# Performance work log

Hardware: AMD Instinct MI355X
Metric: run time of the kernel (lower is better)

The kernel has to match this reference:

```python
import jax, jax.numpy as jnp
import numpy as np

EMBED = 768
HEADS = 12
FACTOR = 2
LN_EPS = 1e-5


def layer_norm(x, gamma, beta):
    mu = jnp.mean(x, axis=-1, keepdims=True)
    var = jnp.mean(jnp.square(x - mu), axis=-1, keepdims=True)
    return (x - mu) * jax.lax.rsqrt(var + LN_EPS) * gamma + beta


def setup_inputs() -> dict:
    key = jax.random.key(0)
    ks = jax.random.split(key, 8)
    B, S, E = 8, 1024, EMBED
    H = FACTOR * E
    s_e = 1.0 / np.sqrt(E)
    s_h = 1.0 / np.sqrt(H)
    return {
        "x": jax.random.normal(ks[0], (B, S, E), jnp.float32),
        "Wq": jax.random.normal(ks[1], (E, E), jnp.float32) * s_e,
        "Wk": jax.random.normal(ks[2], (E, E), jnp.float32) * s_e,
        "Wv": jax.random.normal(ks[3], (E, E), jnp.float32) * s_e,
        "W1": jax.random.normal(ks[4], (E, H), jnp.float32) * s_e,
        "b1": jnp.zeros((H,), jnp.float32),
        "W2": jax.random.normal(ks[5], (H, E), jnp.float32) * s_h,
        "b2": jnp.zeros((E,), jnp.float32),
        "g1": jnp.ones((E,), jnp.float32),
        "beta1": jnp.zeros((E,), jnp.float32),
        "g2": jnp.ones((E,), jnp.float32),
        "beta2": jnp.zeros((E,), jnp.float32),
    }


def reference(x, Wq, Wk, Wv, W1, b1, W2, b2, g1, beta1, g2, beta2):
    B, S, E = x.shape
    hd = E // HEADS
    # NOTE: original reshapes (B,S,E)->(B,H,S,hd) WITHOUT transposing heads
    # (non-standard: mixes sequence blocks across heads) - replicated faithfully.
    q = (x @ Wq).reshape(B, HEADS, S, hd)
    k = (x @ Wk).reshape(B, HEADS, S, hd)
    v = (x @ Wv).reshape(B, HEADS, S, hd)
    # no 1/sqrt(d) scaling in the original
    attn = jax.nn.softmax(jnp.einsum('bnqd,bnkd->bnqk', q, k), axis=-1)
    # NOTE: original einsum 'bnqk,bnvd->bnqd' sums over BOTH k and v
    # (value is sum-pooled over its sequence axis) - replicated faithfully.
    out = jnp.einsum('bnqk,bnvd->bnqd', attn, v)
    out = out.transpose(0, 2, 1, 3).reshape(B, S, E)
    a = x + layer_norm(out, g1, beta1)
    # GELU after BOTH linears (exact GELU, torch default)
    h = jax.nn.gelu(a @ W1 + b1, approximate=False)
    m = jax.nn.gelu(h @ W2 + b2, approximate=False)
    return x + layer_norm(m, g2, beta2)
```

## Files before the change

### kernel.cpp

```cpp
#include <hip/hip_runtime.h>
#include <hip/hip_bf16.h>
#include <math.h>

#define E_ 768
#define HID_ 1536
#define SQ_ 1024

typedef unsigned short u16;
using bf16x8 = __attribute__((ext_vector_type(8))) __bf16;
using f32x4  = __attribute__((ext_vector_type(4))) float;

__device__ __forceinline__ u16 f2bf(float f) {
  union { float f; unsigned u; } v; v.f = f;
  unsigned r = v.u + 0x7FFFu + ((v.u >> 16) & 1u);
  return (u16)(r >> 16);
}
__device__ __forceinline__ float bf2f(u16 h) {
  union { unsigned u; float f; } v; v.u = ((unsigned)h) << 16; return v.f;
}
__device__ __forceinline__ float gelu_f(float x) {
  return 0.5f * x * (1.0f + erff(x * 0.70710678118654752f));
}

#define GLDS16(gp, sp) __builtin_amdgcn_global_load_lds( \
    (__attribute__((address_space(1))) const void*)(const void*)(gp), \
    (__attribute__((address_space(3))) void*)(void*)(sp), 16, 0, 0)

__global__ void prep_kernel(const float* __restrict__ x, const float* __restrict__ W1,
                            const float* __restrict__ W2, u16* __restrict__ xb,
                            u16* __restrict__ W1T, u16* __restrict__ W2T) {
  __shared__ float T[64 * 65];
  int bid = blockIdx.x, t = threadIdx.x;
  if (bid < 6144) {
    int base = bid * 1024 + t * 4;
    const float4 v = *reinterpret_cast<const float4*>(x + base);
    ushort4 o; o.x = f2bf(v.x); o.y = f2bf(v.y); o.z = f2bf(v.z); o.w = f2bf(v.w);
    *reinterpret_cast<ushort4*>(xb + base) = o;
    return;
  }
  const float* in; u16* out; int R_in, C_in, rt, ct;
  if (bid < 6432) {
    int b2 = bid - 6144; in = W1; out = W1T; R_in = 768; C_in = 1536;
    rt = b2 / 24; ct = b2 % 24;
  } else {
    int b3 = bid - 6432; in = W2; out = W2T; R_in = 1536; C_in = 768;
    rt = b3 / 12; ct = b3 % 12;
  }
  int r0 = rt << 6, c0 = ct << 6;
  int tr = t >> 4, tc4 = (t & 15) << 2;
#pragma unroll
  for (int i = 0; i < 4; ++i) {
    int row = tr + (i << 4);
    const float4 v = *reinterpret_cast<const float4*>(in + (size_t)(r0 + row) * C_in + c0 + tc4);
    T[row * 65 + tc4 + 0] = v.x;
    T[row * 65 + tc4 + 1] = v.y;
    T[row * 65 + tc4 + 2] = v.z;
    T[row * 65 + tc4 + 3] = v.w;
  }
  __syncthreads();
#pragma unroll
  for (int i = 0; i < 4; ++i) {
    int orow = tr + (i << 4);
    ushort4 o;
    o.x = f2bf(T[(tc4 + 0) * 65 + orow]);
    o.y = f2bf(T[(tc4 + 1) * 65 + orow]);
    o.z = f2bf(T[(tc4 + 2) * 65 + orow]);
    o.w = f2bf(T[(tc4 + 3) * 65 + orow]);
    *reinterpret_cast<ushort4*>(out + (size_t)(c0 + orow) * R_in + r0 + tc4) = o;
  }
}

__global__ void rowsum_kernel(const u16* __restrict__ xb, float* __restrict__ Rp,
                              float* __restrict__ Y) {
  int bid = blockIdx.x;
  int r = bid >> 2, c = bid & 3;
  int b = r / 12, n = r % 12;
  int t = threadIdx.x;
  if (bid == 0) {
#pragma unroll
    for (int i = 0; i < 24; ++i) Y[t + i * 256] = 0.f;
  }
  int u0 = n << 10;
  int s_lo = u0 / 12;
  int s_hi = (u0 + 1023) / 12;
  int cnt = s_hi - s_lo + 1;
  int cs = s_lo + (cnt * c) / 4;
  int ce = s_lo + (cnt * (c + 1)) / 4;
  float acc[12][3];
#pragma unroll
  for (int g = 0; g < 12; ++g)
    for (int q = 0; q < 3; ++q) acc[g][q] = 0.f;
  const u16* xp = xb + (size_t)b * SQ_ * E_;
  for (int s = cs; s < ce; ++s) {
    float v0 = bf2f(xp[(size_t)s * E_ + t]);
    float v1 = bf2f(xp[(size_t)s * E_ + t + 256]);
    float v2 = bf2f(xp[(size_t)s * E_ + t + 512]);
    int du = 12 * s - u0;
#pragma unroll
    for (int g = 0; g < 12; ++g) {
      int u = du + g;
      if (u >= 0 && u < 1024) { acc[g][0] += v0; acc[g][1] += v1; acc[g][2] += v2; }
    }
  }
  float* Rr = Rp + (size_t)bid * 9216;
#pragma unroll
  for (int g = 0; g < 12; ++g) {
    Rr[g * 768 + t]       = acc[g][0];
    Rr[g * 768 + t + 256] = acc[g][1];
    Rr[g * 768 + t + 512] = acc[g][2];
  }
}

__global__ __launch_bounds__(256, 4) void yfin_kernel(
    const float* __restrict__ Rp, const float* __restrict__ Wv,
    float* __restrict__ Y) {
  int bid = blockIdx.x;
  int r = bid >> 2, jq = bid & 3;
  int t = threadIdx.x;
  __shared__ float Ls[12 * 192];
  __shared__ float red[4][12][64];
  const float* Rb = Rp + (size_t)r * 4 * 9216 + jq * 192;
  for (int i = t; i < 576; i += 256) {
    int g = i / 48, off = (i % 48) << 2;
    const float* p = Rb + g * 768 + off;
    float4 v0 = *reinterpret_cast<const float4*>(p);
    float4 v1 = *reinterpret_cast<const float4*>(p + 9216);
    float4 v2 = *reinterpret_cast<const float4*>(p + 18432);
    float4 v3 = *reinterpret_cast<const float4*>(p + 27648);
    float4 s4;
    s4.x = (v0.x + v1.x) + (v2.x + v3.x);
    s4.y = (v0.y + v1.y) + (v2.y + v3.y);
    s4.z = (v0.z + v1.z) + (v2.z + v3.z);
    s4.w = (v0.w + v1.w) + (v2.w + v3.w);
    *reinterpret_cast<float4*>(&Ls[g * 192 + off]) = s4;
  }
  __syncthreads();
  int d = t & 63, sub = t >> 6;
  float part[12];
#pragma unroll
  for (int g = 0; g < 12; ++g) part[g] = 0.f;
  int jl0 = sub * 48;
  const float* wp = Wv + (size_t)(jq * 192) * 768 + d;
  for (int jj = 0; jj < 48; ++jj) {
    int jl = jl0 + jj;
    const float* wj = wp + (size_t)jl * 768;
#pragma unroll
    for (int g = 0; g < 12; ++g)
      part[g] += Ls[g * 192 + jl] * wj[g * 64];
  }
#pragma unroll
  for (int g = 0; g < 12; ++g) red[sub][g][d] = part[g];
  __syncthreads();
  if (t < 64) {
    float s = 0.f;
#pragma unroll
    for (int su = 0; su < 4; ++su)
#pragma unroll
      for (int g = 0; g < 12; ++g) s += red[su][g][t];
    atomicAdd(&Y[r * 64 + t], s);
  }
}

__global__ void c1_kernel(const float* __restrict__ Y, const float* __restrict__ g1,
                          const float* __restrict__ be1, const float* __restrict__ W1,
                          const float* __restrict__ b1, float* __restrict__ C1) {
  int bid = blockIdx.x;
  int b = bid / 48, c = bid % 48;
  int t = threadIdx.x;
  __shared__ float Ls[768];
  __shared__ float red[8][32];
  __shared__ float red2[8];
  float y0 = Y[b * 768 + t];
  float y1 = Y[b * 768 + t + 256];
  float y2 = Y[b * 768 + t + 512];
  float s = y0 + y1 + y2;
  float sq = y0 * y0 + y1 * y1 + y2 * y2;
#pragma unroll
  for (int o = 32; o > 0; o >>= 1) { s += __shfl_down(s, o, 64); sq += __shfl_down(sq, o, 64); }
  if ((t & 63) == 0) { red2[(t >> 6) * 2] = s; red2[(t >> 6) * 2 + 1] = sq; }
  __syncthreads();
  s  = red2[0] + red2[2] + red2[4] + red2[6];
  sq = red2[1] + red2[3] + red2[5] + red2[7];
  float mu = s * (1.f / 768.f);
  float var = sq * (1.f / 768.f) - mu * mu;
  float rsv = rsqrtf(var + 1e-5f);
  Ls[t]       = (y0 - mu) * rsv * g1[t]       + be1[t];
  Ls[t + 256] = (y1 - mu) * rsv * g1[t + 256] + be1[t + 256];
  Ls[t + 512] = (y2 - mu) * rsv * g1[t + 512] + be1[t + 512];
  __syncthreads();
  int tc = t & 31, ts = t >> 5;
  int n = c * 32 + tc;
  float acc = 0.f;
  int j0 = ts * 96;
#pragma unroll 4
  for (int j = j0; j < j0 + 96; ++j) acc += Ls[j] * W1[(size_t)j * HID_ + n];
  red[ts][tc] = acc;
  __syncthreads();
  if (ts == 0) {
    float sv = b1[n];
#pragma unroll
    for (int k = 0; k < 8; ++k) sv += red[k][tc];
    C1[b * HID_ + n] = sv;
  }
}

template <int MODE>
__global__ __launch_bounds__(256, 2) void gemm_bt_kernel(
    const u16* __restrict__ A, const u16* __restrict__ BT,
    const float* __restrict__ bias, void* __restrict__ out0, void* __restrict__ out1,
    int N, int lda, int ldb) {
  __shared__ __align__(16) u16 As[128 * 64];
  __shared__ __align__(16) u16 Bs[128 * 64];
  int bid = blockIdx.x;
  int xcd = bid & 7, idx = bid >> 3;
  int mloc, n_, k_off, kk = 0;
  if (MODE == 0) { mloc = idx / 12; n_ = idx % 12; k_off = 0; }
  else           { kk = idx / 48; int rem = idx % 48; mloc = rem / 6; n_ = rem % 6; k_off = kk * 768; }
  int bm = (xcd * 8 + mloc) << 7, bn = n_ << 7;

  int t = threadIdx.x;
  int lane = t & 63, w = t >> 6;
  int wm = (w >> 1) << 6, wn = (w & 1) << 6;
  int quad = lane >> 4, l16 = lane & 15;
  f32x4 acc[4][4] = {};

  for (int k0 = 0; k0 < 768; k0 += 64) {
    __syncthreads();
#pragma unroll
    for (int i = 0; i < 4; ++i) {
      int ci = t + (i << 8);
      int r = ci >> 3, csw = ci & 7;
      int kc = csw ^ (r & 7);
      const u16* ga = A + (size_t)(bm + r) * lda + k_off + k0 + (kc << 3);
      GLDS16(ga, As + ci * 8);
      const u16* gb = BT + (size_t)(bn + r) * ldb + k_off + k0 + (kc << 3);
      GLDS16(gb, Bs + ci * 8);
    }
    __builtin_amdgcn_s_waitcnt(0);
    __syncthreads();
#pragma unroll
    for (int ks = 0; ks < 2; ++ks) {
      bf16x8 af[4], bf[4];
      int kc = (ks << 2) + quad;
#pragma unroll
      for (int mt = 0; mt < 4; ++mt) {
        int row = wm + (mt << 4) + l16;
        af[mt] = *reinterpret_cast<const bf16x8*>(As + row * 64 + ((kc ^ (row & 7)) << 3));
      }
#pragma unroll
      for (int nt = 0; nt < 4; ++nt) {
        int row = wn + (nt << 4) + l16;
        bf[nt] = *reinterpret_cast<const bf16x8*>(Bs + row * 64 + ((kc ^ (row & 7)) << 3));
      }
#pragma unroll
      for (int mt = 0; mt < 4; ++mt)
#pragma unroll
        for (int nt = 0; nt < 4; ++nt)
          acc[mt][nt] = __builtin_amdgcn_mfma_f32_16x16x32_bf16(af[mt], bf[nt], acc[mt][nt], 0, 0, 0);
    }
  }

#pragma unroll
  for (int mt = 0; mt < 4; ++mt) {
    int row0 = bm + wm + (mt << 4) + (quad << 2);
#pragma unroll
    for (int nt = 0; nt < 4; ++nt) {
      int col = bn + wn + (nt << 4) + l16;
      float bv = (MODE == 0) ? bias[(bm >> 10) * N + col] : 0.f;
#pragma unroll
      for (int rr = 0; rr < 4; ++rr) {
        float v = acc[mt][nt][rr] + bv;
        size_t idxo = (size_t)(row0 + rr) * N + col;
        if (MODE == 0)       ((u16*)out0)[idxo] = f2bf(gelu_f(v));
        else if (kk == 0)    ((u16*)out0)[idxo] = f2bf(v);
        else                 ((u16*)out1)[idxo] = f2bf(v);
      }
    }
  }
}

__global__ void ln2_kernel(const u16* __restrict__ p0, const u16* __restrict__ p1,
                           const float* __restrict__ x, const float* __restrict__ b2,
                           const float* __restrict__ g2, const float* __restrict__ be2,
                           float* __restrict__ out) {
  int row = blockIdx.x, t = threadIdx.x;
  int e = t << 2;
  ushort4 pa = *reinterpret_cast<const ushort4*>(p0 + (size_t)row * 768 + e);
  ushort4 pb = *reinterpret_cast<const ushort4*>(p1 + (size_t)row * 768 + e);
  float4 bb = *reinterpret_cast<const float4*>(b2 + e);
  float v0 = gelu_f(bf2f(pa.x) + bf2f(pb.x) + bb.x);
  float v1 = gelu_f(bf2f(pa.y) + bf2f(pb.y) + bb.y);
  float v2 = gelu_f(bf2f(pa.z) + bf2f(pb.z) + bb.z);
  float v3 = gelu_f(bf2f(pa.w) + bf2f(pb.w) + bb.w);
  float s = (v0 + v1) + (v2 + v3);
  float sq = (v0 * v0 + v1 * v1) + (v2 * v2 + v3 * v3);
  __shared__ float red[8];
#pragma unroll
  for (int o = 32; o > 0; o >>= 1) { s += __shfl_down(s, o, 64); sq += __shfl_down(sq, o, 64); }
  if ((t & 63) == 0) { red[(t >> 6) * 2] = s; red[(t >> 6) * 2 + 1] = sq; }
  __syncthreads();
  s  = red[0] + red[2] + red[4];
  sq = red[1] + red[3] + red[5];
  float mu = s * (1.f / 768.f);
  float var = sq * (1.f / 768.f) - mu * mu;
  float rs = rsqrtf(var + 1e-5f);
  float4 gg = *reinterpret_cast<const float4*>(g2 + e);
  float4 be = *reinterpret_cast<const float4*>(be2 + e);
  float4 xx = *reinterpret_cast<const float4*>(x + (size_t)row * 768 + e);
  float4 o;
  o.x = xx.x + (v0 - mu) * rs * gg.x + be.x;
  o.y = xx.y + (v1 - mu) * rs * gg.y + be.y;
  o.z = xx.z + (v2 - mu) * rs * gg.z + be.z;
  o.w = xx.w + (v3 - mu) * rs * gg.w + be.w;
  *reinterpret_cast<float4*>(out + (size_t)row * 768 + e) = o;
}

extern "C" void kernel_launch(void* const* d_in, const int* in_sizes, int n_in,
                              void* d_out, int out_size, void* d_ws, size_t ws_size,
                              hipStream_t stream) {
  const float* x   = (const float*)d_in[0];
  const float* Wv  = (const float*)d_in[3];
  const float* W1  = (const float*)d_in[4];
  const float* b1  = (const float*)d_in[5];
  const float* W2  = (const float*)d_in[6];
  const float* b2  = (const float*)d_in[7];
  const float* g1  = (const float*)d_in[8];
  const float* be1 = (const float*)d_in[9];
  const float* g2  = (const float*)d_in[10];
  const float* be2 = (const float*)d_in[11];
  float* out = (float*)d_out;

  char* ws = (char*)d_ws;
  u16*   xb  = (u16*)(ws);
  u16*   W1T = (u16*)(ws + 12582912);
  u16*   W2T = (u16*)(ws + 14942208);
  u16*   h   = (u16*)(ws + 17301504);
  float* Rp  = (float*)(ws + 17301504);
  float* Y   = (float*)(ws + 44826624);
  float* C1  = (float*)(ws + 44875776);
  u16*   m0  = (u16*)(ws + 44924928);
  u16*   p1  = xb;

  prep_kernel<<<6720, 256, 0, stream>>>(x, W1, W2, xb, W1T, W2T);
  rowsum_kernel<<<384, 256, 0, stream>>>(xb, Rp, Y);
  yfin_kernel<<<384, 256, 0, stream>>>(Rp, Wv, Y);
  c1_kernel<<<384, 256, 0, stream>>>(Y, g1, be1, W1, b1, C1);
  gemm_bt_kernel<0><<<768, 256, 0, stream>>>(xb, W1T, C1, (void*)h, nullptr, 1536, 768, 768);
  gemm_bt_kernel<1><<<768, 256, 0, stream>>>(h, W2T, nullptr, (void*)m0, (void*)p1, 768, 1536, 1536);
  ln2_kernel<<<8192, 192, 0, stream>>>(m0, p1, x, b2, g2, be2, out);
}
```

Measured before the change: 219.0 us.

## Fuse rowsum into prep kernel and c1 bias computation into first GEMM

Moves the per-head row-sum work into extra blocks of the prep kernel, reading fp32 x directly instead of the bf16 copy, and computes the LayerNorm1 plus W1 bias vector inside each first-GEMM block rather than in a separate c1 kernel. This removes two kernel launches and the C1 round trip through global memory. In exchange, every GEMM0 block recomputes LN over Y and a 768x128 matvec against W1 before its main loop, which adds redundant work and prologue latency. Reading x in fp32 also changes the rowsum numerics slightly, making them closer to the reference.

```diff
diff --git a/kernel.cpp b/kernel.cpp
--- a/kernel.cpp
+++ b/kernel.cpp
@@ -28,9 +28,49 @@
 
 __global__ void prep_kernel(const float* __restrict__ x, const float* __restrict__ W1,
                             const float* __restrict__ W2, u16* __restrict__ xb,
-                            u16* __restrict__ W1T, u16* __restrict__ W2T) {
+                            u16* __restrict__ W1T, u16* __restrict__ W2T,
+                            float* __restrict__ Rp, float* __restrict__ Y) {
   __shared__ float T[64 * 65];
   int bid = blockIdx.x, t = threadIdx.x;
+  if (bid >= 6720) {
+    int rb = bid - 6720;
+    int r = rb >> 2, c = rb & 3;
+    int b = r / 12, n = r % 12;
+    if (rb == 0) {
+#pragma unroll
+      for (int i = 0; i < 24; ++i) Y[t + i * 256] = 0.f;
+    }
+    int u0 = n << 10;
+    int s_lo = u0 / 12;
+    int s_hi = (u0 + 1023) / 12;
+    int cnt = s_hi - s_lo + 1;
+    int cs = s_lo + (cnt * c) / 4;
+    int ce = s_lo + (cnt * (c + 1)) / 4;
+    float acc[12][3];
+#pragma unroll
+    for (int g = 0; g < 12; ++g)
+      for (int q = 0; q < 3; ++q) acc[g][q] = 0.f;
+    const float* xp = x + (size_t)b * SQ_ * E_;
+    for (int s = cs; s < ce; ++s) {
+      float v0 = xp[(size_t)s * E_ + t];
+      float v1 = xp[(size_t)s * E_ + t + 256];
+      float v2 = xp[(size_t)s * E_ + t + 512];
+      int du = 12 * s - u0;
+#pragma unroll
+      for (int g = 0; g < 12; ++g) {
+        int u = du + g;
+        if (u >= 0 && u < 1024) { acc[g][0] += v0; acc[g][1] += v1; acc[g][2] += v2; }
+      }
+    }
+    float* Rr = Rp + (size_t)rb * 9216;
+#pragma unroll
+    for (int g = 0; g < 12; ++g) {
+      Rr[g * 768 + t]       = acc[g][0];
+      Rr[g * 768 + t + 256] = acc[g][1];
+      Rr[g * 768 + t + 512] = acc[g][2];
+    }
+    return;
+  }
   if (bid < 6144) {
     int base = bid * 1024 + t * 4;
     const float4 v = *reinterpret_cast<const float4*>(x + base);
@@ -67,47 +107,6 @@
     o.z = f2bf(T[(tc4 + 2) * 65 + orow]);
     o.w = f2bf(T[(tc4 + 3) * 65 + orow]);
     *reinterpret_cast<ushort4*>(out + (size_t)(c0 + orow) * R_in + r0 + tc4) = o;
-  }
-}
-
-__global__ void rowsum_kernel(const u16* __restrict__ xb, float* __restrict__ Rp,
-                              float* __restrict__ Y) {
-  int bid = blockIdx.x;
-  int r = bid >> 2, c = bid & 3;
-  int b = r / 12, n = r % 12;
-  int t = threadIdx.x;
-  if (bid == 0) {
-#pragma unroll
-    for (int i = 0; i < 24; ++i) Y[t + i * 256] = 0.f;
-  }
-  int u0 = n << 10;
-  int s_lo = u0 / 12;
-  int s_hi = (u0 + 1023) / 12;
-  int cnt = s_hi - s_lo + 1;
-  int cs = s_lo + (cnt * c) / 4;
-  int ce = s_lo + (cnt * (c + 1)) / 4;
-  float acc[12][3];
-#pragma unroll
-  for (int g = 0; g < 12; ++g)
-    for (int q = 0; q < 3; ++q) acc[g][q] = 0.f;
-  const u16* xp = xb + (size_t)b * SQ_ * E_;
-  for (int s = cs; s < ce; ++s) {
-    float v0 = bf2f(xp[(size_t)s * E_ + t]);
-    float v1 = bf2f(xp[(size_t)s * E_ + t + 256]);
-    float v2 = bf2f(xp[(size_t)s * E_ + t + 512]);
-    int du = 12 * s - u0;
-#pragma unroll
-    for (int g = 0; g < 12; ++g) {
-      int u = du + g;
-      if (u >= 0 && u < 1024) { acc[g][0] += v0; acc[g][1] += v1; acc[g][2] += v2; }
-    }
-  }
-  float* Rr = Rp + (size_t)bid * 9216;
-#pragma unroll
-  for (int g = 0; g < 12; ++g) {
-    Rr[g * 768 + t]       = acc[g][0];
-    Rr[g * 768 + t + 256] = acc[g][1];
-    Rr[g * 768 + t + 512] = acc[g][2];
   }
 }
 
@@ -161,56 +160,20 @@
   }
 }
 
-__global__ void c1_kernel(const float* __restrict__ Y, const float* __restrict__ g1,
-                          const float* __restrict__ be1, const float* __restrict__ W1,
-                          const float* __restrict__ b1, float* __restrict__ C1) {
-  int bid = blockIdx.x;
-  int b = bid / 48, c = bid % 48;
-  int t = threadIdx.x;
-  __shared__ float Ls[768];
-  __shared__ float red[8][32];
-  __shared__ float red2[8];
-  float y0 = Y[b * 768 + t];
-  float y1 = Y[b * 768 + t + 256];
-  float y2 = Y[b * 768 + t + 512];
-  float s = y0 + y1 + y2;
-  float sq = y0 * y0 + y1 * y1 + y2 * y2;
-#pragma unroll
-  for (int o = 32; o > 0; o >>= 1) { s += __shfl_down(s, o, 64); sq += __shfl_down(sq, o, 64); }
-  if ((t & 63) == 0) { red2[(t >> 6) * 2] = s; red2[(t >> 6) * 2 + 1] = sq; }
-  __syncthreads();
-  s  = red2[0] + red2[2] + red2[4] + red2[6];
-  sq = red2[1] + red2[3] + red2[5] + red2[7];
-  float mu = s * (1.f / 768.f);
-  float var = sq * (1.f / 768.f) - mu * mu;
-  float rsv = rsqrtf(var + 1e-5f);
-  Ls[t]       = (y0 - mu) * rsv * g1[t]       + be1[t];
-  Ls[t + 256] = (y1 - mu) * rsv * g1[t + 256] + be1[t + 256];
-  Ls[t + 512] = (y2 - mu) * rsv * g1[t + 512] + be1[t + 512];
-  __syncthreads();
-  int tc = t & 31, ts = t >> 5;
-  int n = c * 32 + tc;
-  float acc = 0.f;
-  int j0 = ts * 96;
-#pragma unroll 4
-  for (int j = j0; j < j0 + 96; ++j) acc += Ls[j] * W1[(size_t)j * HID_ + n];
-  red[ts][tc] = acc;
-  __syncthreads();
-  if (ts == 0) {
-    float sv = b1[n];
-#pragma unroll
-    for (int k = 0; k < 8; ++k) sv += red[k][tc];
-    C1[b * HID_ + n] = sv;
-  }
-}
-
 template <int MODE>
 __global__ __launch_bounds__(256, 2) void gemm_bt_kernel(
     const u16* __restrict__ A, const u16* __restrict__ BT,
-    const float* __restrict__ bias, void* __restrict__ out0, void* __restrict__ out1,
+    const float* __restrict__ Yv, const float* __restrict__ g1,
+    const float* __restrict__ be1, const float* __restrict__ W1f,
+    const float* __restrict__ b1,
+    void* __restrict__ out0, void* __restrict__ out1,
     int N, int lda, int ldb) {
   __shared__ __align__(16) u16 As[128 * 64];
   __shared__ __align__(16) u16 Bs[128 * 64];
+  __shared__ float Lsc[768];
+  __shared__ float c1s[128];
+  __shared__ float redc[2][128];
+  __shared__ float red2g[8];
   int bid = blockIdx.x;
   int xcd = bid & 7, idx = bid >> 3;
   int mloc, n_, k_off, kk = 0;
@@ -223,6 +186,40 @@
   int wm = (w >> 1) << 6, wn = (w & 1) << 6;
   int quad = lane >> 4, l16 = lane & 15;
   f32x4 acc[4][4] = {};
+
+  if (MODE == 0) {
+    int b = bm >> 10;
+    float y0 = Yv[b * 768 + t];
+    float y1 = Yv[b * 768 + t + 256];
+    float y2 = Yv[b * 768 + t + 512];
+    float s = y0 + y1 + y2;
+    float sq = y0 * y0 + y1 * y1 + y2 * y2;
+#pragma unroll
+    for (int o = 32; o > 0; o >>= 1) { s += __shfl_down(s, o, 64); sq += __shfl_down(sq, o, 64); }
+    if ((t & 63) == 0) { red2g[(t >> 6) * 2] = s; red2g[(t >> 6) * 2 + 1] = sq; }
+    __syncthreads();
+    s  = red2g[0] + red2g[2] + red2g[4] + red2g[6];
+    sq = red2g[1] + red2g[3] + red2g[5] + red2g[7];
+    float mu = s * (1.f / 768.f);
+    float var = sq * (1.f / 768.f) - mu * mu;
+    float rsv = rsqrtf(var + 1e-5f);
+    Lsc[t]       = (y0 - mu) * rsv * g1[t]       + be1[t];
+    Lsc[t + 256] = (y1 - mu) * rsv * g1[t + 256] + be1[t + 256];
+    Lsc[t + 512] = (y2 - mu) * rsv * g1[t + 512] + be1[t + 512];
+    __syncthreads();
+    int col = t & 127, half = t >> 7;
+    float a0 = 0.f, a1 = 0.f;
+    int j0 = half * 384;
+    const float* wc = W1f + bn + col;
+#pragma unroll 4
+    for (int j = j0; j < j0 + 384; j += 2) {
+      a0 += Lsc[j]     * wc[(size_t)j * HID_];
+      a1 += Lsc[j + 1] * wc[(size_t)(j + 1) * HID_];
+    }
+    redc[half][col] = a0 + a1;
+    __syncthreads();
+    if (t < 128) c1s[t] = b1[bn + t] + redc[0][t] + redc[1][t];
+  }
 
   for (int k0 = 0; k0 < 768; k0 += 64) {
     __syncthreads();
@@ -265,8 +262,9 @@
     int row0 = bm + wm + (mt << 4) + (quad << 2);
 #pragma unroll
     for (int nt = 0; nt < 4; ++nt) {
-      int col = bn + wn + (nt << 4) + l16;
-      float bv = (MODE == 0) ? bias[(bm >> 10) * N + col] : 0.f;
+      int cloc = wn + (nt << 4) + l16;
+      int col = bn + cloc;
+      float bv = (MODE == 0) ? c1s[cloc] : 0.f;
 #pragma unroll
       for (int rr = 0; rr < 4; ++rr) {
         float v = acc[mt][nt][rr] + bv;
@@ -337,15 +335,14 @@
   u16*   h   = (u16*)(ws + 17301504);
   float* Rp  = (float*)(ws + 17301504);
   float* Y   = (float*)(ws + 44826624);
-  float* C1  = (float*)(ws + 44875776);
-  u16*   m0  = (u16*)(ws + 44924928);
+  u16*   m0  = (u16*)(ws + 44875776);
   u16*   p1  = xb;
 
-  prep_kernel<<<6720, 256, 0, stream>>>(x, W1, W2, xb, W1T, W2T);
-  rowsum_kernel<<<384, 256, 0, stream>>>(xb, Rp, Y);
+  prep_kernel<<<7104, 256, 0, stream>>>(x, W1, W2, xb, W1T, W2T, Rp, Y);
   yfin_kernel<<<384, 256, 0, stream>>>(Rp, Wv, Y);
-  c1_kernel<<<384, 256, 0, stream>>>(Y, g1, be1, W1, b1, C1);
-  gemm_bt_kernel<0><<<768, 256, 0, stream>>>(xb, W1T, C1, (void*)h, nullptr, 1536, 768, 768);
-  gemm_bt_kernel<1><<<768, 256, 0, stream>>>(h, W2T, nullptr, (void*)m0, (void*)p1, 768, 1536, 1536);
+  gemm_bt_kernel<0><<<768, 256, 0, stream>>>(xb, W1T, Y, g1, be1, W1, b1,
+                                             (void*)h, nullptr, 1536, 768, 768);
+  gemm_bt_kernel<1><<<768, 256, 0, stream>>>(h, W2T, nullptr, nullptr, nullptr, nullptr, nullptr,
+                                             (void*)m0, (void*)p1, 768, 1536, 1536);
   ln2_kernel<<<8192, 192, 0, stream>>>(m0, p1, x, b2, g2, be2, out);
 }
```

Result: no change. 219.2 us (+0.1%).
